# Kernel optimization log

Hardware: AMD Instinct MI355X
Metric: run time of the kernel (lower is better)

## Reference

```python
import jax, jax.numpy as jnp
import numpy as np
from math import sqrt

MIN_SCORE = 0.05
MAX_OVERLAP = 0.45
TOP_K = 200


def make_priors():
    feature_dims = {'mid': 18, 'end': 9, 'a': 9, 'b': 5, 'c': 3, 'd': 1}
    obj_scales = {'mid': 0.2, 'end': 0.2, 'a': 0.375, 'b': 0.55, 'c': 0.725, 'd': 0.9}
    aspect_ratio = {'mid': [1.0, 2.0, 3.0, 0.5, 0.333], 'end': [1.0, 2.0, 3.0, 0.5, 0.333],
                    'a': [1.0, 2.0, 3.0, 0.5, 0.333], 'b': [1.0, 2.0, 3.0, 0.5, 0.333],
                    'c': [1.0, 2.0, 0.5], 'd': [1.0, 2.0, 0.5]}
    fmaps = list(feature_dims.keys())
    boxes = []
    for k, fmap in enumerate(fmaps):
        for i in range(feature_dims[fmap]):
            for j in range(feature_dims[fmap]):
                cx = (j + 0.5) / feature_dims[fmap]
                cy = (i + 0.5) / feature_dims[fmap]
                for ratio in aspect_ratio[fmap]:
                    boxes.append([cx, cy, obj_scales[fmap] * sqrt(ratio), obj_scales[fmap] / sqrt(ratio)])
                if fmap in ['mid', 'end', 'a', 'b', 'c']:
                    s = sqrt(obj_scales[fmap] * obj_scales[fmaps[k + 1]])
                else:
                    s = 1.0
                boxes.append([cx, cy, s, s])
    return np.clip(np.asarray(boxes, dtype=np.float32), 0.0, 1.0)  # [3106, 4]


def setup_inputs() -> dict:
    key = jax.random.key(0)
    k1, k2 = jax.random.split(key)
    return {
        'predicted_locs': jax.random.normal(k1, (4, 3106, 4), dtype=jnp.float32),
        'predicted_scores': jax.random.normal(k2, (4, 3106, 21), dtype=jnp.float32),
        'priors_cxcy': jnp.asarray(make_priors()),
    }


def _decode(predicted_locs, priors):
    # gcxgcy_to_cxcy then cxcy_to_xy (standard SSD variances 0.1 / 0.2)
    cxcy = predicted_locs[..., :2] * priors[..., 2:] / 10.0 + priors[..., :2]
    wh = jnp.exp(predicted_locs[..., 2:] / 5.0) * priors[..., 2:]
    return jnp.concatenate([cxcy - wh / 2.0, cxcy + wh / 2.0], axis=-1)  # xyxy


def _detect_image(boxes_i, probs_i):
    # boxes_i: [P,4] xyxy, probs_i: [P,C] softmax scores
    P = boxes_i.shape[0]
    C = probs_i.shape[1]
    # full pairwise Jaccard overlap [P,P]
    lt = jnp.maximum(boxes_i[:, None, :2], boxes_i[None, :, :2])
    rb = jnp.minimum(boxes_i[:, None, 2:], boxes_i[None, :, 2:])
    inter = jnp.prod(jnp.clip(rb - lt, 0.0), axis=-1)
    area = jnp.prod(boxes_i[:, 2:] - boxes_i[:, :2], axis=-1)
    iou = inter / (area[:, None] + area[None, :] - inter)

    cls = probs_i[:, 1:].T                      # [C-1, P], skip background
    valid = cls > MIN_SCORE
    order = jnp.argsort(-jnp.where(valid, cls, -jnp.inf), axis=1)  # [C-1, P]
    valid_s = jnp.take_along_axis(valid, order, axis=1)
    iou_sg = jax.lax.stop_gradient(iou)

    def body(i, suppress):                       # greedy NMS over sorted boxes, all classes at once
        bi = order[:, i]                         # [C-1] prior index per class
        rows = jnp.take_along_axis(iou_sg[bi], order, axis=1) > MAX_OVERLAP  # [C-1, P]
        skip = suppress[:, i] | ~valid_s[:, i]
        proc = (suppress | rows).at[:, i].set(False)
        return jnp.where(skip[:, None], suppress, proc)

    suppress = jax.lax.fori_loop(0, P, body, ~valid_s)
    keep = ~suppress                             # [C-1, P] (sorted order)

    scores_s = jnp.take_along_axis(cls, order, axis=1)
    cand_scores = jnp.where(keep, scores_s, -jnp.inf).reshape(-1)     # [(C-1)*P]
    cand_boxes = boxes_i[order].reshape(-1, 4)
    cand_labels = jnp.broadcast_to(jnp.arange(1, C, dtype=jnp.int32)[:, None], (C - 1, P)).reshape(-1)

    top_scores, top_idx = jax.lax.top_k(cand_scores, TOP_K)
    top_boxes = cand_boxes[top_idx]
    top_labels = cand_labels[top_idx]

    has = jnp.isfinite(top_scores)
    top_scores = jnp.where(has, top_scores, 0.0)
    top_boxes = jnp.where(has[:, None], top_boxes, 0.0)
    top_labels = jnp.where(has, top_labels, 0)
    count = jnp.minimum(jnp.sum(keep).astype(jnp.int32), TOP_K)

    # torch fallback: a single background box when nothing is detected
    none = count == 0
    top_boxes = top_boxes.at[0].set(jnp.where(none, jnp.array([0.0, 0.0, 1.0, 1.0], dtype=top_boxes.dtype), top_boxes[0]))
    count = jnp.where(none, jnp.int32(1), count)
    return top_boxes, top_labels, top_scores, count


def reference(predicted_locs, predicted_scores, priors_cxcy):
    probs = jax.nn.softmax(predicted_scores, axis=2)          # [B,P,C]
    boxes = _decode(predicted_locs, priors_cxcy[None])        # [B,P,4]
    all_boxes, all_labels, all_scores, counts = jax.vmap(_detect_image)(boxes, probs)
    return all_boxes, all_labels, all_scores, counts
```

## Files before the change

### kernel.cpp

```cpp
#include <hip/hip_runtime.h>

#define NB 4
#define NPRI 3106
#define NC 21
#define NCLS 20
#define KMAX 200
#define NMAX 1024
#define WMAX 16
#define TMAX (WMAX*(WMAX+1)/2)
#define MIN_SC 0.05f
#define MAX_OV 0.45f

#define F_PROBS 0
#define F_KEYS  (F_PROBS + NB*NCLS*NPRI)
#define F_BOXES (F_KEYS + NB*NCLS*NMAX*2)
#define F_AREAS (F_BOXES + NB*NCLS*NMAX*4)
#define F_NCAND (F_AREAS + NB*NCLS*NMAX)
#define F_M     (F_NCAND + 128)
#define F_POOL  (F_M + NB*NCLS*WMAX*NMAX*2)
#define F_CNT   (F_POOL + NB*NCLS*KMAX*2)
#define F_DONE  (F_CNT + NB*NCLS)

#define OUT_BOXES  0
#define OUT_LABELS (NB*KMAX*4)
#define OUT_SCORES (OUT_LABELS + NB*KMAX)
#define OUT_COUNTS (OUT_SCORES + NB*KMAX)

__device__ __forceinline__ float bcast(float v, int l) {
    return __uint_as_float(__builtin_amdgcn_readlane(__float_as_uint(v), l));
}

__device__ __forceinline__ void decode_box(const float* __restrict__ locs,
                                           const float* __restrict__ priors,
                                           int b, int pi,
                                           float& x1, float& y1, float& x2, float& y2) {
    const float* l  = locs + ((size_t)b * NPRI + pi) * 4;
    const float* pr = priors + (size_t)pi * 4;
    float pcx = pr[0], pcy = pr[1], pw = pr[2], ph = pr[3];
    float cx = l[0] * pw / 10.0f + pcx;
    float cy = l[1] * ph / 10.0f + pcy;
    float w  = expf(l[2] / 5.0f) * pw;
    float h  = expf(l[3] / 5.0f) * ph;
    x1 = cx - w / 2.0f;  y1 = cy - h / 2.0f;
    x2 = cx + w / 2.0f;  y2 = cy + h / 2.0f;
}

__global__ __launch_bounds__(256)
void det_softmax(const float* __restrict__ scores, float* __restrict__ ws) {
    __shared__ float row[256 * NC];
    const int t0 = blockIdx.x * 256;
    int items = NB * NPRI - t0; if (items > 256) items = 256;
    const int cntf = items * NC;
    for (int i = threadIdx.x; i < cntf; i += 256)
        row[i] = scores[(size_t)t0 * NC + i];
    __syncthreads();
    const int t = t0 + threadIdx.x;
    if (t >= NB * NPRI) return;
    const int b = t / NPRI, p = t - b * NPRI;
    const float* s = row + threadIdx.x * NC;
    float m = -1e30f;
    #pragma unroll
    for (int c = 0; c < NC; ++c) m = fmaxf(m, s[c]);
    float e[NC]; float sum = 0.0f;
    #pragma unroll
    for (int c = 0; c < NC; ++c) { e[c] = expf(s[c] - m); sum += e[c]; }
    #pragma unroll
    for (int c = 1; c < NC; ++c)
        ws[F_PROBS + ((size_t)(b * NCLS + (c - 1)) * NPRI + p)] = e[c] / sum;
}

__global__ __launch_bounds__(256)
void det_prep(const float* __restrict__ locs, const float* __restrict__ priors,
              float* __restrict__ ws) {
    const int bc  = blockIdx.x;
    const int b   = bc / NCLS;
    const int tid = threadIdx.x;

    __shared__ unsigned long long keys[NMAX];
    __shared__ int n_sh;
    if (tid == 0) n_sh = 0;
    __syncthreads();

    const float* prob = ws + F_PROBS + (size_t)bc * NPRI;
    for (int p = tid; p < NPRI; p += 256) {
        float s = prob[p];
        if (s > MIN_SC) {
            int idx = atomicAdd(&n_sh, 1);
            if (idx < NMAX) {
                unsigned int sb = __float_as_uint(s);
                keys[idx] = ((unsigned long long)(~sb) << 32) | (unsigned int)p;
            }
        }
    }
    __syncthreads();
    int n = n_sh; if (n > NMAX) n = NMAX;

    int npow = 1; while (npow < n) npow <<= 1;
    for (int i = n + tid; i < npow; i += 256) keys[i] = ~0ull;
    for (int k = 2; k <= npow; k <<= 1) {
        for (int j = k >> 1; j > 0; j >>= 1) {
            __syncthreads();
            for (int i = tid; i < npow; i += 256) {
                int ixj = i ^ j;
                if (ixj > i) {
                    unsigned long long a = keys[i], d = keys[ixj];
                    bool up = ((i & k) == 0);
                    if ((a > d) == up) { keys[i] = d; keys[ixj] = a; }
                }
            }
        }
    }
    __syncthreads();

    if (tid == 0) ((int*)(ws + F_NCAND))[bc] = n;
    unsigned long long* gk = (unsigned long long*)(ws + F_KEYS) + (size_t)bc * NMAX;
    float4* gb = (float4*)(ws + F_BOXES) + (size_t)bc * NMAX;
    float*  ga = ws + F_AREAS + (size_t)bc * NMAX;
    for (int i = tid; i < n; i += 256) {
        unsigned long long k = keys[i];
        gk[i] = k;
        int pi = (int)(k & 0xFFFFFFFFull);
        float x1, y1, x2, y2;
        decode_box(locs, priors, b, pi, x1, y1, x2, y2);
        gb[i] = make_float4(x1, y1, x2, y2);
        ga[i] = (x2 - x1) * (y2 - y1);
    }
}

__global__ __launch_bounds__(256)
void det_mbuild(float* __restrict__ ws) {
    if (blockIdx.x == 0 && blockIdx.y == 0 && threadIdx.x < NB)
        ((int*)(ws + F_DONE))[threadIdx.x] = 0;

    const int bc = blockIdx.y;
    const int t  = blockIdx.x * 4 + (threadIdx.x >> 6);
    if (t >= TMAX) return;
    const int lane = threadIdx.x & 63;
    int tj = 0;
    while ((tj + 1) * (tj + 2) / 2 <= t) ++tj;
    const int w = t - tj * (tj + 1) / 2;
    const int n = ((const int*)(ws + F_NCAND))[bc];
    const int bi0 = w * 64, bj0 = tj * 64;
    if (bj0 >= n) return;

    const float4* bx = (const float4*)(ws + F_BOXES) + (size_t)bc * NMAX;
    const float*  ar = ws + F_AREAS + (size_t)bc * NMAX;
    const float4 bi = bx[bi0 + lane];
    const float  ai = ar[bi0 + lane];
    const float4 bj = bx[bj0 + lane];
    const float  aj = ar[bj0 + lane];
    const unsigned long long vm =
        (n - bi0 >= 64) ? ~0ull : ((1ull << (n - bi0)) - 1ull);
    const bool diag = (w == tj);
    unsigned long long myword = 0ull;

    #pragma unroll
    for (int jj = 0; jj < 64; jj += 2) {
        float ax1 = bcast(bj.x, jj),     ay1 = bcast(bj.y, jj);
        float ax2 = bcast(bj.z, jj),     ay2 = bcast(bj.w, jj);
        float aau = bcast(aj, jj);
        float bx1 = bcast(bj.x, jj + 1), by1 = bcast(bj.y, jj + 1);
        float bx2 = bcast(bj.z, jj + 1), by2 = bcast(bj.w, jj + 1);
        float bau = bcast(aj, jj + 1);

        float alx = fmaxf(bi.x, ax1), aly = fmaxf(bi.y, ay1);
        float arx = fminf(bi.z, ax2), ary = fminf(bi.w, ay2);
        float blx = fmaxf(bi.x, bx1), bly = fmaxf(bi.y, by1);
        float brx = fminf(bi.z, bx2), bry = fminf(bi.w, by2);
        float adx = fmaxf(arx - alx, 0.0f), ady = fmaxf(ary - aly, 0.0f);
        float bdx = fmaxf(brx - blx, 0.0f), bdy = fmaxf(bry - bly, 0.0f);
        float ain = adx * ady;
        float bin = bdx * bdy;
        float au  = ai + aau - ain;
        float bu  = ai + bau - bin;
        float at  = MAX_OV * au;
        float bt  = MAX_OV * bu;
        bool akeep = ain > at;
        bool bkeep = bin > bt;
        bool anear = fabsf(ain - at) <= at * 6e-7f;
        bool bnear = fabsf(bin - bt) <= bt * 6e-7f;
        if (__ballot(anear || bnear)) {
            float aio = ain / au;
            float bio = bin / bu;
            akeep = anear ? (aio > MAX_OV) : akeep;
            bkeep = bnear ? (bio > MAX_OV) : bkeep;
        }
        unsigned long long abits = __ballot(akeep) & vm;
        unsigned long long bbits = __ballot(bkeep) & vm;
        if (diag) {
            abits &= (1ull << jj) - 1ull;
            bbits &= (1ull << (jj + 1)) - 1ull;
        }
        if (lane == jj)     myword = abits;
        if (lane == jj + 1) myword = bbits;
    }
    if (bj0 + lane < n)
        ((unsigned long long*)(ws + F_M))
            [((size_t)bc * WMAX + w) * NMAX + bj0 + lane] = myword;
}

__global__ __launch_bounds__(256)
void det_finish(const float* __restrict__ locs, const float* __restrict__ priors,
                float* __restrict__ ws, float* __restrict__ out) {
    const int bc   = blockIdx.x;
    const int b    = bc / NCLS;
    const int c    = bc - b * NCLS;
    const int cls  = c + 1;
    const int tid  = threadIdx.x;
    int* done_i = (int*)(ws + F_DONE);

    if (tid < 64) {
        const int lane = tid;
        const int n    = ((const int*)(ws + F_NCAND))[bc];
        const unsigned long long* Mb =
            (const unsigned long long*)(ws + F_M) + (size_t)bc * WMAX * NMAX;

        unsigned long long kw[WMAX];
        #pragma unroll
        for (int w = 0; w < WMAX; ++w) kw[w] = 0ull;

        const unsigned long long lmask = (1ull << lane) - 1ull;
        #pragma unroll
        for (int w = 0; w < WMAX; ++w) {
            if (w * 64 < n) {
                int cc = w * 64 + lane;
                bool valid = cc < n;
                unsigned long long pre = 0ull;
                #pragma unroll
                for (int v = 0; v < WMAX; ++v)
                    if (v < w) pre |= Mb[(size_t)v * NMAX + cc] & kw[v];
                unsigned long long dg = Mb[(size_t)w * NMAX + cc] & lmask;
                bool sup0 = (pre != 0ull);
                unsigned long long K = __ballot(valid && !sup0);
                for (int it = 0; it < 64; ++it) {
                    bool sup = sup0 || ((dg & K) != 0ull);
                    unsigned long long Kn = __ballot(valid && !sup);
                    if (Kn == K) break;
                    K = Kn;
                }
                kw[w] = K;
            }
        }

        int pref[WMAX + 1];
        pref[0] = 0;
        #pragma unroll
        for (int w = 0; w < WMAX; ++w) pref[w + 1] = pref[w] + __popcll(kw[w]);
        if (lane == 0) ((int*)(ws + F_CNT))[bc] = pref[WMAX];

        const unsigned long long* gk =
            (const unsigned long long*)(ws + F_KEYS) + (size_t)bc * NMAX;
        unsigned long long* pool =
            (unsigned long long*)(ws + F_POOL) + (size_t)bc * KMAX;
        const unsigned long long ctag = (unsigned long long)(cls << 12);
        #pragma unroll
        for (int w = 0; w < WMAX; ++w) {
            unsigned long long kwv = kw[w];
            int cc = w * 64 + lane;
            if (cc < n && ((kwv >> lane) & 1ull)) {
                int pos = pref[w] + __popcll(kwv & lmask);
                if (pos < KMAX) pool[pos] = gk[cc] | ctag;
            }
        }
    }

    {
        int idx = c * 256 + tid;
        if (idx < KMAX * 4) {
            out[OUT_BOXES + (size_t)b * KMAX * 4 + idx] = 0.0f;
        } else if (idx < KMAX * 4 + KMAX) {
            out[OUT_LABELS + b * KMAX + (idx - KMAX * 4)] = 0.0f;
        } else if (idx < KMAX * 4 + 2 * KMAX) {
            out[OUT_SCORES + b * KMAX + (idx - KMAX * 4 - KMAX)] = 0.0f;
        }
    }

    __threadfence();
    __syncthreads();
    if (tid == 0)
        __hip_atomic_fetch_add(done_i + b, 1, __ATOMIC_RELEASE,
                               __HIP_MEMORY_SCOPE_AGENT);

    if (tid == 0) {
        int it = 0;
        while (__hip_atomic_load(done_i + b, __ATOMIC_ACQUIRE,
                                 __HIP_MEMORY_SCOPE_AGENT) < NCLS
               && it < (1 << 20)) ++it;
    }
    __syncthreads();

    __shared__ unsigned long long lpool[NCLS * KMAX];
    __shared__ int cnts[NCLS];

    const int* cnt = (const int*)(ws + F_CNT);
    if (tid < NCLS) cnts[tid] = cnt[b * NCLS + tid];
    __syncthreads();

    const unsigned long long* pool =
        (const unsigned long long*)(ws + F_POOL) + (size_t)b * NCLS * KMAX;
    for (int i = tid; i < NCLS * KMAX; i += 256) {
        int c2 = i / KMAX, r = i - c2 * KMAX;
        int mc2 = cnts[c2] < KMAX ? cnts[c2] : KMAX;
        lpool[i] = (r < mc2) ? pool[i] : ~0ull;
    }
    __syncthreads();

    if (c == 0 && tid == 0) {
        int tot = 0;
        for (int c2 = 0; c2 < NCLS; ++c2) tot += cnts[c2];
        int count = tot < KMAX ? tot : KMAX;
        if (tot == 0) {
            float* ob = out + OUT_BOXES + (size_t)b * KMAX * 4;
            ob[0] = 0.0f; ob[1] = 0.0f; ob[2] = 1.0f; ob[3] = 1.0f;
            count = 1;
        }
        out[OUT_COUNTS + b] = (float)count;
    }

    const int mc = cnts[c] < KMAX ? cnts[c] : KMAX;
    if (tid < mc) {
        unsigned long long key = lpool[c * KMAX + tid];
        int rank = 0;
        #pragma unroll
        for (int c2 = 0; c2 < NCLS; ++c2) {
            int lo = 0, hi = KMAX;
            #pragma unroll
            for (int s = 0; s < 8; ++s) {
                int mid = (lo + hi) >> 1;
                int midc = mid < KMAX ? mid : KMAX - 1;
                unsigned long long v = lpool[c2 * KMAX + midc];
                bool lt = (lo < hi) && (v < key);
                lo = lt ? mid + 1 : lo;
                hi = lt ? hi : mid;
            }
            rank += lo;
        }
        if (rank < KMAX) {
            unsigned int lo32 = (unsigned int)key;
            int pi  = lo32 & 0xFFF;
            int lab = (lo32 >> 12) & 0x1F;
            float sc = __uint_as_float(~(unsigned int)(key >> 32));
            float x1, y1, x2, y2;
            decode_box(locs, priors, b, pi, x1, y1, x2, y2);
            float* ob = out + OUT_BOXES + ((size_t)b * KMAX + rank) * 4;
            ob[0] = x1; ob[1] = y1; ob[2] = x2; ob[3] = y2;
            out[OUT_LABELS + b * KMAX + rank] = (float)lab;
            out[OUT_SCORES + b * KMAX + rank] = sc;
        }
    }
}

extern "C" void kernel_launch(void* const* d_in, const int* in_sizes, int n_in,
                              void* d_out, int out_size, void* d_ws, size_t ws_size,
                              hipStream_t stream) {
    const float* locs   = (const float*)d_in[0];
    const float* scores = (const float*)d_in[1];
    const float* priors = (const float*)d_in[2];
    float* out = (float*)d_out;
    float* ws  = (float*)d_ws;

    det_softmax<<<(NB * NPRI + 255) / 256, 256, 0, stream>>>(scores, ws);
    det_prep<<<NB * NCLS, 256, 0, stream>>>(locs, priors, ws);
    det_mbuild<<<dim3((TMAX + 3) / 4, NB * NCLS), 256, 0, stream>>>(ws);
    det_finish<<<NB * NCLS, 256, 0, stream>>>(locs, priors, ws, out);
}
```

Measured before the change: 174.2 us.

## Fuse softmax into prep and merge mask build with finish via atomic counters

Softmax is recomputed per (batch,class) block inside det_prep, which removes the separate softmax kernel and its probability round-trip through global memory. Each block redundantly reads all scores for its image and computes the full softmax. The mask-build and finish kernels are merged into one grid: the build blocks signal completion through a per-class atomic counter, and an extra block per class spin-waits on that counter before running the NMS finish. This cuts two launches but relies on the build blocks being scheduled alongside the waiting block, and the spin is bounded by an iteration cap.

```diff
diff --git a/kernel.cpp b/kernel.cpp
--- a/kernel.cpp
+++ b/kernel.cpp
@@ -8,10 +8,12 @@
 #define NMAX 1024
 #define WMAX 16
 #define TMAX (WMAX*(WMAX+1)/2)
+#define TBLK (TMAX/4)
 #define MIN_SC 0.05f
 #define MAX_OV 0.45f
 
 #define F_PROBS 0
+#define F_TDONE F_PROBS
 #define F_KEYS  (F_PROBS + NB*NCLS*NPRI)
 #define F_BOXES (F_KEYS + NB*NCLS*NMAX*2)
 #define F_AREAS (F_BOXES + NB*NCLS*NMAX*4)
@@ -45,62 +47,63 @@
     x2 = cx + w / 2.0f;  y2 = cy + h / 2.0f;
 }
 
-__global__ __launch_bounds__(256)
-void det_softmax(const float* __restrict__ scores, float* __restrict__ ws) {
-    __shared__ float row[256 * NC];
-    const int t0 = blockIdx.x * 256;
-    int items = NB * NPRI - t0; if (items > 256) items = 256;
-    const int cntf = items * NC;
-    for (int i = threadIdx.x; i < cntf; i += 256)
-        row[i] = scores[(size_t)t0 * NC + i];
-    __syncthreads();
-    const int t = t0 + threadIdx.x;
-    if (t >= NB * NPRI) return;
-    const int b = t / NPRI, p = t - b * NPRI;
-    const float* s = row + threadIdx.x * NC;
-    float m = -1e30f;
-    #pragma unroll
-    for (int c = 0; c < NC; ++c) m = fmaxf(m, s[c]);
-    float e[NC]; float sum = 0.0f;
-    #pragma unroll
-    for (int c = 0; c < NC; ++c) { e[c] = expf(s[c] - m); sum += e[c]; }
-    #pragma unroll
-    for (int c = 1; c < NC; ++c)
-        ws[F_PROBS + ((size_t)(b * NCLS + (c - 1)) * NPRI + p)] = e[c] / sum;
-}
-
-__global__ __launch_bounds__(256)
-void det_prep(const float* __restrict__ locs, const float* __restrict__ priors,
-              float* __restrict__ ws) {
+__global__ __launch_bounds__(512)
+void det_prep(const float* __restrict__ scores, const float* __restrict__ locs,
+              const float* __restrict__ priors, float* __restrict__ ws) {
     const int bc  = blockIdx.x;
     const int b   = bc / NCLS;
+    const int c   = bc - b * NCLS;
     const int tid = threadIdx.x;
 
+    __shared__ float rows[512 * NC];
     __shared__ unsigned long long keys[NMAX];
     __shared__ int n_sh;
-    if (tid == 0) n_sh = 0;
-    __syncthreads();
-
-    const float* prob = ws + F_PROBS + (size_t)bc * NPRI;
-    for (int p = tid; p < NPRI; p += 256) {
-        float s = prob[p];
-        if (s > MIN_SC) {
-            int idx = atomicAdd(&n_sh, 1);
-            if (idx < NMAX) {
-                unsigned int sb = __float_as_uint(s);
-                keys[idx] = ((unsigned long long)(~sb) << 32) | (unsigned int)p;
-            }
-        }
-    }
-    __syncthreads();
+    if (tid == 0) {
+        n_sh = 0;
+        ((int*)(ws + F_TDONE))[bc] = 0;
+        if (c == 0) ((int*)(ws + F_DONE))[b] = 0;
+    }
+    __syncthreads();
+
+    const float* sbase = scores + (size_t)b * NPRI * NC;
+    for (int base = 0; base < NPRI; base += 512) {
+        int cnt = NPRI - base; if (cnt > 512) cnt = 512;
+        const int tot = cnt * NC;
+        for (int i = tid; i < tot; i += 512)
+            rows[i] = sbase[(size_t)base * NC + i];
+        __syncthreads();
+        if (tid < cnt) {
+            const float* s = rows + tid * NC;
+            float m = -1e30f;
+            #pragma unroll
+            for (int k = 0; k < NC; ++k) m = fmaxf(m, s[k]);
+            float sum = 0.0f, ec = 0.0f;
+            #pragma unroll
+            for (int k = 0; k < NC; ++k) {
+                float e = expf(s[k] - m);
+                sum += e;
+                if (k == c + 1) ec = e;
+            }
+            float val = ec / sum;
+            if (val > MIN_SC) {
+                int idx = atomicAdd(&n_sh, 1);
+                if (idx < NMAX) {
+                    unsigned int sb = __float_as_uint(val);
+                    keys[idx] = ((unsigned long long)(~sb) << 32)
+                              | (unsigned int)(base + tid);
+                }
+            }
+        }
+        __syncthreads();
+    }
     int n = n_sh; if (n > NMAX) n = NMAX;
 
     int npow = 1; while (npow < n) npow <<= 1;
-    for (int i = n + tid; i < npow; i += 256) keys[i] = ~0ull;
+    for (int i = n + tid; i < npow; i += 512) keys[i] = ~0ull;
     for (int k = 2; k <= npow; k <<= 1) {
         for (int j = k >> 1; j > 0; j >>= 1) {
             __syncthreads();
-            for (int i = tid; i < npow; i += 256) {
+            for (int i = tid; i < npow; i += 512) {
                 int ixj = i ^ j;
                 if (ixj > i) {
                     unsigned long long a = keys[i], d = keys[ixj];
@@ -116,7 +119,7 @@
     unsigned long long* gk = (unsigned long long*)(ws + F_KEYS) + (size_t)bc * NMAX;
     float4* gb = (float4*)(ws + F_BOXES) + (size_t)bc * NMAX;
     float*  ga = ws + F_AREAS + (size_t)bc * NMAX;
-    for (int i = tid; i < n; i += 256) {
+    for (int i = tid; i < n; i += 512) {
         unsigned long long k = keys[i];
         gk[i] = k;
         int pi = (int)(k & 0xFFFFFFFFull);
@@ -127,87 +130,97 @@
     }
 }
 
-__global__ __launch_bounds__(256)
-void det_mbuild(float* __restrict__ ws) {
-    if (blockIdx.x == 0 && blockIdx.y == 0 && threadIdx.x < NB)
-        ((int*)(ws + F_DONE))[threadIdx.x] = 0;
-
+__global__ __launch_bounds__(256, 4)
+void det_build_finish(const float* __restrict__ locs, const float* __restrict__ priors,
+                      float* __restrict__ ws, float* __restrict__ out) {
     const int bc = blockIdx.y;
-    const int t  = blockIdx.x * 4 + (threadIdx.x >> 6);
-    if (t >= TMAX) return;
-    const int lane = threadIdx.x & 63;
-    int tj = 0;
-    while ((tj + 1) * (tj + 2) / 2 <= t) ++tj;
-    const int w = t - tj * (tj + 1) / 2;
-    const int n = ((const int*)(ws + F_NCAND))[bc];
-    const int bi0 = w * 64, bj0 = tj * 64;
-    if (bj0 >= n) return;
-
-    const float4* bx = (const float4*)(ws + F_BOXES) + (size_t)bc * NMAX;
-    const float*  ar = ws + F_AREAS + (size_t)bc * NMAX;
-    const float4 bi = bx[bi0 + lane];
-    const float  ai = ar[bi0 + lane];
-    const float4 bj = bx[bj0 + lane];
-    const float  aj = ar[bj0 + lane];
-    const unsigned long long vm =
-        (n - bi0 >= 64) ? ~0ull : ((1ull << (n - bi0)) - 1ull);
-    const bool diag = (w == tj);
-    unsigned long long myword = 0ull;
-
-    #pragma unroll
-    for (int jj = 0; jj < 64; jj += 2) {
-        float ax1 = bcast(bj.x, jj),     ay1 = bcast(bj.y, jj);
-        float ax2 = bcast(bj.z, jj),     ay2 = bcast(bj.w, jj);
-        float aau = bcast(aj, jj);
-        float bx1 = bcast(bj.x, jj + 1), by1 = bcast(bj.y, jj + 1);
-        float bx2 = bcast(bj.z, jj + 1), by2 = bcast(bj.w, jj + 1);
-        float bau = bcast(aj, jj + 1);
-
-        float alx = fmaxf(bi.x, ax1), aly = fmaxf(bi.y, ay1);
-        float arx = fminf(bi.z, ax2), ary = fminf(bi.w, ay2);
-        float blx = fmaxf(bi.x, bx1), bly = fmaxf(bi.y, by1);
-        float brx = fminf(bi.z, bx2), bry = fminf(bi.w, by2);
-        float adx = fmaxf(arx - alx, 0.0f), ady = fmaxf(ary - aly, 0.0f);
-        float bdx = fmaxf(brx - blx, 0.0f), bdy = fmaxf(bry - bly, 0.0f);
-        float ain = adx * ady;
-        float bin = bdx * bdy;
-        float au  = ai + aau - ain;
-        float bu  = ai + bau - bin;
-        float at  = MAX_OV * au;
-        float bt  = MAX_OV * bu;
-        bool akeep = ain > at;
-        bool bkeep = bin > bt;
-        bool anear = fabsf(ain - at) <= at * 6e-7f;
-        bool bnear = fabsf(bin - bt) <= bt * 6e-7f;
-        if (__ballot(anear || bnear)) {
-            float aio = ain / au;
-            float bio = bin / bu;
-            akeep = anear ? (aio > MAX_OV) : akeep;
-            bkeep = bnear ? (bio > MAX_OV) : bkeep;
-        }
-        unsigned long long abits = __ballot(akeep) & vm;
-        unsigned long long bbits = __ballot(bkeep) & vm;
-        if (diag) {
-            abits &= (1ull << jj) - 1ull;
-            bbits &= (1ull << (jj + 1)) - 1ull;
-        }
-        if (lane == jj)     myword = abits;
-        if (lane == jj + 1) myword = bbits;
-    }
-    if (bj0 + lane < n)
-        ((unsigned long long*)(ws + F_M))
-            [((size_t)bc * WMAX + w) * NMAX + bj0 + lane] = myword;
-}
-
-__global__ __launch_bounds__(256)
-void det_finish(const float* __restrict__ locs, const float* __restrict__ priors,
-                float* __restrict__ ws, float* __restrict__ out) {
-    const int bc   = blockIdx.x;
+    int* tdone = (int*)(ws + F_TDONE);
+
+    if (blockIdx.x < TBLK) {
+        const int t    = blockIdx.x * 4 + (threadIdx.x >> 6);
+        const int lane = threadIdx.x & 63;
+        int tj = 0;
+        while ((tj + 1) * (tj + 2) / 2 <= t) ++tj;
+        const int w = t - tj * (tj + 1) / 2;
+        const int n = ((const int*)(ws + F_NCAND))[bc];
+        const int bi0 = w * 64, bj0 = tj * 64;
+        if (bj0 < n) {
+            const float4* bx = (const float4*)(ws + F_BOXES) + (size_t)bc * NMAX;
+            const float*  ar = ws + F_AREAS + (size_t)bc * NMAX;
+            const float4 bi = bx[bi0 + lane];
+            const float  ai = ar[bi0 + lane];
+            const float4 bj = bx[bj0 + lane];
+            const float  aj = ar[bj0 + lane];
+            const unsigned long long vm =
+                (n - bi0 >= 64) ? ~0ull : ((1ull << (n - bi0)) - 1ull);
+            const bool diag = (w == tj);
+            unsigned long long myword = 0ull;
+
+            #pragma unroll
+            for (int jj = 0; jj < 64; jj += 2) {
+                float ax1 = bcast(bj.x, jj),     ay1 = bcast(bj.y, jj);
+                float ax2 = bcast(bj.z, jj),     ay2 = bcast(bj.w, jj);
+                float aau = bcast(aj, jj);
+                float bx1 = bcast(bj.x, jj + 1), by1 = bcast(bj.y, jj + 1);
+                float bx2 = bcast(bj.z, jj + 1), by2 = bcast(bj.w, jj + 1);
+                float bau = bcast(aj, jj + 1);
+
+                float alx = fmaxf(bi.x, ax1), aly = fmaxf(bi.y, ay1);
+                float arx = fminf(bi.z, ax2), ary = fminf(bi.w, ay2);
+                float blx = fmaxf(bi.x, bx1), bly = fmaxf(bi.y, by1);
+                float brx = fminf(bi.z, bx2), bry = fminf(bi.w, by2);
+                float adx = fmaxf(arx - alx, 0.0f), ady = fmaxf(ary - aly, 0.0f);
+                float bdx = fmaxf(brx - blx, 0.0f), bdy = fmaxf(bry - bly, 0.0f);
+                float ain = adx * ady;
+                float bin = bdx * bdy;
+                float au  = ai + aau - ain;
+                float bu  = ai + bau - bin;
+                float at  = MAX_OV * au;
+                float bt  = MAX_OV * bu;
+                bool akeep = ain > at;
+                bool bkeep = bin > bt;
+                bool anear = fabsf(ain - at) <= at * 6e-7f;
+                bool bnear = fabsf(bin - bt) <= bt * 6e-7f;
+                if (__ballot(anear || bnear)) {
+                    float aio = ain / au;
+                    float bio = bin / bu;
+                    akeep = anear ? (aio > MAX_OV) : akeep;
+                    bkeep = bnear ? (bio > MAX_OV) : bkeep;
+                }
+                unsigned long long abits = __ballot(akeep) & vm;
+                unsigned long long bbits = __ballot(bkeep) & vm;
+                if (diag) {
+                    abits &= (1ull << jj) - 1ull;
+                    bbits &= (1ull << (jj + 1)) - 1ull;
+                }
+                if (lane == jj)     myword = abits;
+                if (lane == jj + 1) myword = bbits;
+            }
+            if (bj0 + lane < n)
+                ((unsigned long long*)(ws + F_M))
+                    [((size_t)bc * WMAX + w) * NMAX + bj0 + lane] = myword;
+        }
+        __threadfence();
+        __syncthreads();
+        if (threadIdx.x == 0)
+            __hip_atomic_fetch_add(tdone + bc, 1, __ATOMIC_RELEASE,
+                                   __HIP_MEMORY_SCOPE_AGENT);
+        return;
+    }
+
     const int b    = bc / NCLS;
     const int c    = bc - b * NCLS;
     const int cls  = c + 1;
     const int tid  = threadIdx.x;
     int* done_i = (int*)(ws + F_DONE);
+
+    if (tid == 0) {
+        int it = 0;
+        while (__hip_atomic_load(tdone + bc, __ATOMIC_ACQUIRE,
+                                 __HIP_MEMORY_SCOPE_AGENT) < TBLK
+               && it < (1 << 20)) ++it;
+    }
+    __syncthreads();
 
     if (tid < 64) {
         const int lane = tid;
@@ -359,8 +372,6 @@
     float* out = (float*)d_out;
     float* ws  = (float*)d_ws;
 
-    det_softmax<<<(NB * NPRI + 255) / 256, 256, 0, stream>>>(scores, ws);
-    det_prep<<<NB * NCLS, 256, 0, stream>>>(locs, priors, ws);
-    det_mbuild<<<dim3((TMAX + 3) / 4, NB * NCLS), 256, 0, stream>>>(ws);
-    det_finish<<<NB * NCLS, 256, 0, stream>>>(locs, priors, ws, out);
-}
+    det_prep<<<NB * NCLS, 512, 0, stream>>>(scores, locs, priors, ws);
+    det_build_finish<<<dim3(TBLK + 1, NB * NCLS), 256, 0, stream>>>(locs, priors, ws, out);
+}
```

After: 375.0 us. +115.3%, slower.
